# Performance work log

Hardware: AMD Instinct MI355X
Metric: run time of the kernel (lower is better)

Reference implementation:

```python
import jax, jax.numpy as jnp
import numpy as np

N_NODES = 100000
N_EDGES = 1600000
HID = 32


def gcn_conv(x, W, b, src, dst, num_nodes):
    # PyG GCNConv: h = X W; out = D^{-1/2}(A+I)D^{-1/2} h + b
    # (self loops already appended to src/dst by caller)
    h = x @ W
    deg = jax.ops.segment_sum(jnp.ones_like(dst, dtype=h.dtype), dst,
                              num_segments=num_nodes)
    dinv = jnp.where(deg > 0, jax.lax.rsqrt(deg), 0.0)
    norm = dinv[src] * dinv[dst]                      # [E+N]
    msg = h[src] * norm[:, None]                      # gather + scale
    out = jax.ops.segment_sum(msg, dst, num_segments=num_nodes)  # scatter-add
    return out + b


def setup_inputs() -> dict:
    key = jax.random.key(0)
    ks = jax.random.split(key, 12)
    x = jax.random.normal(ks[0], (N_NODES, 2), dtype=jnp.float32)
    edge_index = jax.random.randint(ks[1], (2, N_EDGES), 0, N_NODES,
                                    dtype=jnp.int32)
    s = 0.2  # small init scale
    return {
        "x": x,
        "edge_index": edge_index,
        "fc1_W": jax.random.normal(ks[2], (2, HID), jnp.float32) * s,
        "fc1_b": jnp.zeros((HID,), jnp.float32),
        "c1_W": jax.random.normal(ks[3], (HID, HID), jnp.float32) * s,
        "c1_b": jnp.zeros((HID,), jnp.float32),
        "c2_W": jax.random.normal(ks[4], (HID, HID), jnp.float32) * s,
        "c2_b": jnp.zeros((HID,), jnp.float32),
        "c3_W": jax.random.normal(ks[5], (HID, HID), jnp.float32) * s,
        "c3_b": jnp.zeros((HID,), jnp.float32),
        "fc2_W": jax.random.normal(ks[6], (HID, HID), jnp.float32) * s,
        "fc2_b": jnp.zeros((HID,), jnp.float32),
        "fc3_W": jax.random.normal(ks[7], (HID, 1), jnp.float32) * s,
        "fc3_b": jnp.zeros((1,), jnp.float32),
    }


def reference(x, edge_index, fc1_W, fc1_b, c1_W, c1_b, c2_W, c2_b,
              c3_W, c3_b, fc2_W, fc2_b, fc3_W, fc3_b):
    num_nodes = x.shape[0]
    loop = jnp.arange(num_nodes, dtype=edge_index.dtype)
    src = jnp.concatenate([edge_index[0], loop])  # add self loops
    dst = jnp.concatenate([edge_index[1], loop])
    h = jax.nn.relu(x @ fc1_W + fc1_b)
    h = jax.nn.relu(gcn_conv(h, c1_W, c1_b, src, dst, num_nodes))
    h = jax.nn.relu(gcn_conv(h, c2_W, c2_b, src, dst, num_nodes))
    h = jax.nn.relu(gcn_conv(h, c3_W, c3_b, src, dst, num_nodes))
    h = jax.nn.relu(h @ fc2_W + fc2_b)
    return h @ fc3_W + fc3_b
```

## Files before the change

kernel.cpp:

```cpp
#include <hip/hip_runtime.h>

#define NN 100000
#define NE 1600000
#define HID 32
#define NBK 391
#define CAP 4608
#define CHUNK 4096

__global__ __launch_bounds__(256) void partA_kernel(
        const int* __restrict__ src, const int* __restrict__ dst,
        int* __restrict__ bktcur, int* __restrict__ bedges) {
    __shared__ int cache[CHUNK];
    __shared__ int hist[NBK];
    __shared__ int lofs[NBK];
    int t = threadIdx.x;
    int base = blockIdx.x * CHUNK;
    for (int i = t; i < NBK; i += 256) hist[i] = 0;
    __syncthreads();
    for (int i = t; i < CHUNK; i += 256) {
        int e = base + i;
        if (e < NE) {
            int d = dst[e];
            cache[i] = d;
            atomicAdd(&hist[d >> 8], 1);
        }
    }
    __syncthreads();
    for (int i = t; i < NBK; i += 256)
        lofs[i] = hist[i] ? atomicAdd(&bktcur[i], hist[i]) : 0;
    __syncthreads();
    for (int i = t; i < CHUNK; i += 256) {
        int e = base + i;
        if (e < NE) {
            int d = cache[i];
            int s = src[e];
            int b = d >> 8;
            int rel = atomicAdd(&lofs[b], 1);
            if (rel < CAP) bedges[b * CAP + rel] = (s << 8) | (d & 255);
        }
    }
}

__global__ __launch_bounds__(256) void bucket_csr_fc1_kernel(
        const int* __restrict__ bedges, const int* __restrict__ bktcur,
        const float* __restrict__ x, const float* __restrict__ W1,
        const float* __restrict__ b1, float* __restrict__ dinv,
        int* __restrict__ srcidx, int* __restrict__ rbeg, int* __restrict__ rend,
        float* __restrict__ hs) {
    __shared__ int ldeg[256];
    __shared__ int lcur[256];
    __shared__ int wsum[256];
    __shared__ float sdinv[256];
    __shared__ float xs[512];
    __shared__ float wb[96];
    int b = blockIdx.x, t = threadIdx.x;
    int ebeg = b * CAP;
    int cnt = min(bktcur[b], CAP);
    int n0 = b << 8;
    ldeg[t] = 0;
    if (t < 96) wb[t] = (t < 64) ? W1[t] : b1[t - 64];
    for (int i = t; i < 512; i += 256) {
        int gi = 2 * n0 + i;
        xs[i] = (gi < 2 * NN) ? x[gi] : 0.f;
    }
    __syncthreads();
    for (int e = t; e < cnt; e += 256)
        atomicAdd(&ldeg[bedges[ebeg + e] & 255], 1);
    __syncthreads();
    int a = ldeg[t];
    wsum[t] = a;
    __syncthreads();
    for (int off = 1; off < 256; off <<= 1) {
        int xv = (t >= off) ? wsum[t - off] : 0;
        __syncthreads();
        wsum[t] += xv;
        __syncthreads();
    }
    int excl = wsum[t] - a;
    lcur[t] = excl;
    float dv = rsqrtf((float)(a + 1));
    sdinv[t] = dv;
    int n = n0 + t;
    if (n < NN) {
        rbeg[n] = ebeg + excl;
        rend[n] = ebeg + excl + a;
        dinv[n] = dv;
    }
    __syncthreads();
    for (int e = t; e < cnt; e += 256) {
        int w = bedges[ebeg + e];
        int pos = atomicAdd(&lcur[w & 255], 1);
        srcidx[ebeg + pos] = (unsigned)w >> 8;
    }
    int j = t & 31;
#pragma unroll
    for (int r = 0; r < 32; ++r) {
        int ln = (t >> 5) + (r << 3);
        int nn = n0 + ln;
        if (nn < NN) {
            float v = xs[2 * ln] * wb[j] + xs[2 * ln + 1] * wb[32 + j] + wb[64 + j];
            hs[(nn << 5) + j] = fmaxf(v, 0.f) * sdinv[ln];
        }
    }
}

template <bool OUTSCALE>
__global__ void conv_fused_kernel(const float* __restrict__ hs_in,
                                  const int* __restrict__ rbeg,
                                  const int* __restrict__ rend,
                                  const int* __restrict__ srcidx,
                                  const float* __restrict__ dinv,
                                  const float* __restrict__ W,
                                  const float* __restrict__ bias,
                                  float* __restrict__ hs_out) {
    __shared__ float wl[HID * HID];
    __shared__ float agg[8][HID];
    int tid = threadIdx.x;
    int base8 = blockIdx.x * 8;
#pragma unroll
    for (int i = 0; i < 4; ++i) wl[tid + 256 * i] = W[tid + 256 * i];
    int wave = tid >> 6, lane = tid & 63;
    int g = lane >> 3;
    int l = lane & 7;
#pragma unroll
    for (int rep = 0; rep < 2; ++rep) {
        int ln = wave * 2 + rep;
        int n = base8 + ln;
        int beg = rbeg[n], end = rend[n];
        float4 acc0 = make_float4(0.f, 0.f, 0.f, 0.f);
        float4 acc1 = make_float4(0.f, 0.f, 0.f, 0.f);
        int e = beg + g;
        for (; e + 8 < end; e += 16) {
            int s0 = srcidx[e];
            int s1 = srcidx[e + 8];
            float4 v0 = *(const float4*)&hs_in[(s0 << 5) + (l << 2)];
            float4 v1 = *(const float4*)&hs_in[(s1 << 5) + (l << 2)];
            acc0.x += v0.x; acc0.y += v0.y; acc0.z += v0.z; acc0.w += v0.w;
            acc1.x += v1.x; acc1.y += v1.y; acc1.z += v1.z; acc1.w += v1.w;
        }
        if (e < end) {
            int s0 = srcidx[e];
            float4 v0 = *(const float4*)&hs_in[(s0 << 5) + (l << 2)];
            acc0.x += v0.x; acc0.y += v0.y; acc0.z += v0.z; acc0.w += v0.w;
        }
        acc0.x += acc1.x; acc0.y += acc1.y; acc0.z += acc1.z; acc0.w += acc1.w;
#pragma unroll
        for (int m = 8; m < 64; m <<= 1) {
            acc0.x += __shfl_xor(acc0.x, m);
            acc0.y += __shfl_xor(acc0.y, m);
            acc0.z += __shfl_xor(acc0.z, m);
            acc0.w += __shfl_xor(acc0.w, m);
        }
        if (g == 0) {
            float4 self = *(const float4*)&hs_in[(n << 5) + (l << 2)];
            float dv = dinv[n];
            float4 r;
            r.x = (acc0.x + self.x) * dv;
            r.y = (acc0.y + self.y) * dv;
            r.z = (acc0.z + self.z) * dv;
            r.w = (acc0.w + self.w) * dv;
            *(float4*)&agg[ln][l << 2] = r;
        }
    }
    __syncthreads();
    int ln = tid >> 5, j = tid & 31;
    int n = base8 + ln;
    float v = 0.f;
#pragma unroll
    for (int k = 0; k < HID; ++k) v += agg[ln][k] * wl[k * HID + j];
    v = fmaxf(v + bias[j], 0.f);
    if (OUTSCALE) v *= dinv[n];
    hs_out[(n << 5) + j] = v;
}

__global__ void fc23_kernel(const float* __restrict__ h, const float* __restrict__ W2,
                            const float* __restrict__ b2, const float* __restrict__ W3,
                            const float* __restrict__ b3, float* __restrict__ out) {
    __shared__ float wl[HID * HID];
    __shared__ float hsl[256];
    int tid = threadIdx.x;
    int base = blockIdx.x * 256;
#pragma unroll
    for (int i = 0; i < 4; ++i) wl[tid + 256 * i] = W2[tid + 256 * i];
    hsl[tid] = h[base + tid];
    __syncthreads();
    int ln = tid >> 5, j = tid & 31;
    float v = 0.f;
#pragma unroll
    for (int k = 0; k < HID; ++k) v += hsl[ln * HID + k] * wl[k * HID + j];
    v = fmaxf(v + b2[j], 0.f);
    float p = v * W3[j];
#pragma unroll
    for (int m = 16; m; m >>= 1) p += __shfl_xor(p, m);
    if (j == 0) out[(base >> 5) + ln] = p + b3[0];
}

extern "C" void kernel_launch(void* const* d_in, const int* in_sizes, int n_in,
                              void* d_out, int out_size, void* d_ws, size_t ws_size,
                              hipStream_t stream) {
    const float* x     = (const float*)d_in[0];
    const int*   ei    = (const int*)d_in[1];
    const float* fc1_W = (const float*)d_in[2];
    const float* fc1_b = (const float*)d_in[3];
    const float* c1_W  = (const float*)d_in[4];
    const float* c1_b  = (const float*)d_in[5];
    const float* c2_W  = (const float*)d_in[6];
    const float* c2_b  = (const float*)d_in[7];
    const float* c3_W  = (const float*)d_in[8];
    const float* c3_b  = (const float*)d_in[9];
    const float* fc2_W = (const float*)d_in[10];
    const float* fc2_b = (const float*)d_in[11];
    const float* fc3_W = (const float*)d_in[12];
    const float* fc3_b = (const float*)d_in[13];

    const int* src = ei;
    const int* dst = ei + NE;

    float* ws     = (float*)d_ws;
    float* dinv   = ws;
    float* hA     = ws + NN;
    float* hB     = hA + NN * HID;
    int*   srcidx = (int*)(hB + NN * HID);
    int*   rbeg   = srcidx + NBK * CAP;
    int*   rend   = rbeg + NN;
    int*   bktcur = rend + NN;
    int*   bedges = (int*)hB;

    float* out = (float*)d_out;

    const int B = 256;
    const int gNH = (NN * HID) / B;
    const int gPart = (NE + CHUNK - 1) / CHUNK;

    hipMemsetAsync(bktcur, 0, NBK * sizeof(int), stream);
    partA_kernel<<<gPart, B, 0, stream>>>(src, dst, bktcur, bedges);
    bucket_csr_fc1_kernel<<<NBK, B, 0, stream>>>(bedges, bktcur, x, fc1_W, fc1_b,
                                                 dinv, srcidx, rbeg, rend, hA);

    conv_fused_kernel<true><<<gNH, B, 0, stream>>>(hA, rbeg, rend, srcidx, dinv, c1_W, c1_b, hB);
    conv_fused_kernel<true><<<gNH, B, 0, stream>>>(hB, rbeg, rend, srcidx, dinv, c2_W, c2_b, hA);
    conv_fused_kernel<false><<<gNH, B, 0, stream>>>(hA, rbeg, rend, srcidx, dinv, c3_W, c3_b, hB);

    fc23_kernel<<<gNH, B, 0, stream>>>(hB, fc2_W, fc2_b, fc3_W, fc3_b, out);
}
```

Before: 192.5 us.

## Fuse fc1 into first conv gather and fc2/fc3 into last conv

```diff
diff --git a/kernel.cpp b/kernel.cpp
--- a/kernel.cpp
+++ b/kernel.cpp
@@ -5,7 +5,7 @@
 #define HID 32
 #define NBK 391
 #define CAP 4608
-#define CHUNK 4096
+#define CHUNK 8192
 
 __global__ __launch_bounds__(256) void partA_kernel(
         const int* __restrict__ src, const int* __restrict__ dst,
@@ -41,28 +41,19 @@
     }
 }
 
-__global__ __launch_bounds__(256) void bucket_csr_fc1_kernel(
+__global__ __launch_bounds__(256) void bucket_csr_kernel(
         const int* __restrict__ bedges, const int* __restrict__ bktcur,
-        const float* __restrict__ x, const float* __restrict__ W1,
-        const float* __restrict__ b1, float* __restrict__ dinv,
+        const float* __restrict__ x, float* __restrict__ dinv,
         int* __restrict__ srcidx, int* __restrict__ rbeg, int* __restrict__ rend,
-        float* __restrict__ hs) {
+        float4* __restrict__ xpack) {
     __shared__ int ldeg[256];
     __shared__ int lcur[256];
     __shared__ int wsum[256];
-    __shared__ float sdinv[256];
-    __shared__ float xs[512];
-    __shared__ float wb[96];
     int b = blockIdx.x, t = threadIdx.x;
     int ebeg = b * CAP;
     int cnt = min(bktcur[b], CAP);
     int n0 = b << 8;
     ldeg[t] = 0;
-    if (t < 96) wb[t] = (t < 64) ? W1[t] : b1[t - 64];
-    for (int i = t; i < 512; i += 256) {
-        int gi = 2 * n0 + i;
-        xs[i] = (gi < 2 * NN) ? x[gi] : 0.f;
-    }
     __syncthreads();
     for (int e = t; e < cnt; e += 256)
         atomicAdd(&ldeg[bedges[ebeg + e] & 255], 1);
@@ -78,13 +69,14 @@
     }
     int excl = wsum[t] - a;
     lcur[t] = excl;
-    float dv = rsqrtf((float)(a + 1));
-    sdinv[t] = dv;
     int n = n0 + t;
     if (n < NN) {
+        float dv = rsqrtf((float)(a + 1));
         rbeg[n] = ebeg + excl;
         rend[n] = ebeg + excl + a;
         dinv[n] = dv;
+        float2 xv2 = *(const float2*)&x[2 * n];
+        xpack[n] = make_float4(xv2.x, xv2.y, dv, 0.f);
     }
     __syncthreads();
     for (int e = t; e < cnt; e += 256) {
@@ -92,19 +84,83 @@
         int pos = atomicAdd(&lcur[w & 255], 1);
         srcidx[ebeg + pos] = (unsigned)w >> 8;
     }
-    int j = t & 31;
-#pragma unroll
-    for (int r = 0; r < 32; ++r) {
-        int ln = (t >> 5) + (r << 3);
-        int nn = n0 + ln;
-        if (nn < NN) {
-            float v = xs[2 * ln] * wb[j] + xs[2 * ln + 1] * wb[32 + j] + wb[64 + j];
-            hs[(nn << 5) + j] = fmaxf(v, 0.f) * sdinv[ln];
-        }
-    }
-}
-
-template <bool OUTSCALE>
+}
+
+__global__ __launch_bounds__(256) void conv1_kernel(
+        const float4* __restrict__ xpack, const int* __restrict__ rbeg,
+        const int* __restrict__ rend, const int* __restrict__ srcidx,
+        const float* __restrict__ dinv, const float* __restrict__ W1,
+        const float* __restrict__ b1, const float* __restrict__ W,
+        const float* __restrict__ bias, float* __restrict__ hs_out) {
+    __shared__ float wl[HID * HID];
+    __shared__ float agg[8][HID];
+    int tid = threadIdx.x;
+    int base8 = blockIdx.x * 8;
+#pragma unroll
+    for (int i = 0; i < 4; ++i) wl[tid + 256 * i] = W[tid + 256 * i];
+    int wave = tid >> 6, lane = tid & 63;
+    int g = lane >> 3;
+    int l = lane & 7;
+    float4 w0q = *(const float4*)&W1[l << 2];
+    float4 w1q = *(const float4*)&W1[HID + (l << 2)];
+    float4 bq  = *(const float4*)&b1[l << 2];
+#pragma unroll
+    for (int rep = 0; rep < 2; ++rep) {
+        int ln = wave * 2 + rep;
+        int n = base8 + ln;
+        int beg = rbeg[n], end = rend[n];
+        float4 acc0 = make_float4(0.f, 0.f, 0.f, 0.f);
+        float4 acc1 = make_float4(0.f, 0.f, 0.f, 0.f);
+        int e = beg + g;
+        for (; e + 8 < end; e += 16) {
+            float4 p0 = xpack[srcidx[e]];
+            float4 p1 = xpack[srcidx[e + 8]];
+            acc0.x += fmaxf(p0.x * w0q.x + p0.y * w1q.x + bq.x, 0.f) * p0.z;
+            acc0.y += fmaxf(p0.x * w0q.y + p0.y * w1q.y + bq.y, 0.f) * p0.z;
+            acc0.z += fmaxf(p0.x * w0q.z + p0.y * w1q.z + bq.z, 0.f) * p0.z;
+            acc0.w += fmaxf(p0.x * w0q.w + p0.y * w1q.w + bq.w, 0.f) * p0.z;
+            acc1.x += fmaxf(p1.x * w0q.x + p1.y * w1q.x + bq.x, 0.f) * p1.z;
+            acc1.y += fmaxf(p1.x * w0q.y + p1.y * w1q.y + bq.y, 0.f) * p1.z;
+            acc1.z += fmaxf(p1.x * w0q.z + p1.y * w1q.z + bq.z, 0.f) * p1.z;
+            acc1.w += fmaxf(p1.x * w0q.w + p1.y * w1q.w + bq.w, 0.f) * p1.z;
+        }
+        if (e < end) {
+            float4 p0 = xpack[srcidx[e]];
+            acc0.x += fmaxf(p0.x * w0q.x + p0.y * w1q.x + bq.x, 0.f) * p0.z;
+            acc0.y += fmaxf(p0.x * w0q.y + p0.y * w1q.y + bq.y, 0.f) * p0.z;
+            acc0.z += fmaxf(p0.x * w0q.z + p0.y * w1q.z + bq.z, 0.f) * p0.z;
+            acc0.w += fmaxf(p0.x * w0q.w + p0.y * w1q.w + bq.w, 0.f) * p0.z;
+        }
+        acc0.x += acc1.x; acc0.y += acc1.y; acc0.z += acc1.z; acc0.w += acc1.w;
+#pragma unroll
+        for (int m = 8; m < 64; m <<= 1) {
+            acc0.x += __shfl_xor(acc0.x, m);
+            acc0.y += __shfl_xor(acc0.y, m);
+            acc0.z += __shfl_xor(acc0.z, m);
+            acc0.w += __shfl_xor(acc0.w, m);
+        }
+        if (g == 0) {
+            float4 ps = xpack[n];
+            float dv = ps.z;
+            float4 r;
+            r.x = (acc0.x + fmaxf(ps.x * w0q.x + ps.y * w1q.x + bq.x, 0.f) * dv) * dv;
+            r.y = (acc0.y + fmaxf(ps.x * w0q.y + ps.y * w1q.y + bq.y, 0.f) * dv) * dv;
+            r.z = (acc0.z + fmaxf(ps.x * w0q.z + ps.y * w1q.z + bq.z, 0.f) * dv) * dv;
+            r.w = (acc0.w + fmaxf(ps.x * w0q.w + ps.y * w1q.w + bq.w, 0.f) * dv) * dv;
+            *(float4*)&agg[ln][l << 2] = r;
+        }
+    }
+    __syncthreads();
+    int ln = tid >> 5, j = tid & 31;
+    int n = base8 + ln;
+    float v = 0.f;
+#pragma unroll
+    for (int k = 0; k < HID; ++k) v += agg[ln][k] * wl[k * HID + j];
+    v = fmaxf(v + bias[j], 0.f) * dinv[n];
+    hs_out[(n << 5) + j] = v;
+}
+
+template <bool OUTSCALE, bool FUSE23>
 __global__ void conv_fused_kernel(const float* __restrict__ hs_in,
                                   const int* __restrict__ rbeg,
                                   const int* __restrict__ rend,
@@ -112,6 +168,10 @@
                                   const float* __restrict__ dinv,
                                   const float* __restrict__ W,
                                   const float* __restrict__ bias,
+                                  const float* __restrict__ W2,
+                                  const float* __restrict__ b2,
+                                  const float* __restrict__ W3,
+                                  const float* __restrict__ b3,
                                   float* __restrict__ hs_out) {
     __shared__ float wl[HID * HID];
     __shared__ float agg[8][HID];
@@ -170,29 +230,23 @@
     for (int k = 0; k < HID; ++k) v += agg[ln][k] * wl[k * HID + j];
     v = fmaxf(v + bias[j], 0.f);
     if (OUTSCALE) v *= dinv[n];
-    hs_out[(n << 5) + j] = v;
-}
-
-__global__ void fc23_kernel(const float* __restrict__ h, const float* __restrict__ W2,
-                            const float* __restrict__ b2, const float* __restrict__ W3,
-                            const float* __restrict__ b3, float* __restrict__ out) {
-    __shared__ float wl[HID * HID];
-    __shared__ float hsl[256];
-    int tid = threadIdx.x;
-    int base = blockIdx.x * 256;
-#pragma unroll
-    for (int i = 0; i < 4; ++i) wl[tid + 256 * i] = W2[tid + 256 * i];
-    hsl[tid] = h[base + tid];
-    __syncthreads();
-    int ln = tid >> 5, j = tid & 31;
-    float v = 0.f;
-#pragma unroll
-    for (int k = 0; k < HID; ++k) v += hsl[ln * HID + k] * wl[k * HID + j];
-    v = fmaxf(v + b2[j], 0.f);
-    float p = v * W3[j];
-#pragma unroll
-    for (int m = 16; m; m >>= 1) p += __shfl_xor(p, m);
-    if (j == 0) out[(base >> 5) + ln] = p + b3[0];
+    if (!FUSE23) {
+        hs_out[(n << 5) + j] = v;
+    } else {
+        __syncthreads();
+#pragma unroll
+        for (int i = 0; i < 4; ++i) wl[tid + 256 * i] = W2[tid + 256 * i];
+        agg[ln][j] = v;
+        __syncthreads();
+        float v2 = 0.f;
+#pragma unroll
+        for (int k = 0; k < HID; ++k) v2 += agg[ln][k] * wl[k * HID + j];
+        v2 = fmaxf(v2 + b2[j], 0.f);
+        float p = v2 * W3[j];
+#pragma unroll
+        for (int m = 16; m; m >>= 1) p += __shfl_xor(p, m);
+        if (j == 0) hs_out[n] = p + b3[0];
+    }
 }
 
 extern "C" void kernel_launch(void* const* d_in, const int* in_sizes, int n_in,
@@ -216,15 +270,16 @@
     const int* src = ei;
     const int* dst = ei + NE;
 
-    float* ws     = (float*)d_ws;
-    float* dinv   = ws;
-    float* hA     = ws + NN;
-    float* hB     = hA + NN * HID;
-    int*   srcidx = (int*)(hB + NN * HID);
-    int*   rbeg   = srcidx + NBK * CAP;
-    int*   rend   = rbeg + NN;
-    int*   bktcur = rend + NN;
-    int*   bedges = (int*)hB;
+    float*  ws     = (float*)d_ws;
+    float*  dinv   = ws;
+    float*  hA     = ws + NN;
+    float*  hB     = hA + NN * HID;
+    float4* xpack  = (float4*)(hB + NN * HID);
+    int*    srcidx = (int*)(xpack + NN);
+    int*    rbeg   = srcidx + NBK * CAP;
+    int*    rend   = rbeg + NN;
+    int*    bktcur = rend + NN;
+    int*    bedges = (int*)hB;
 
     float* out = (float*)d_out;
 
@@ -234,12 +289,12 @@
 
     hipMemsetAsync(bktcur, 0, NBK * sizeof(int), stream);
     partA_kernel<<<gPart, B, 0, stream>>>(src, dst, bktcur, bedges);
-    bucket_csr_fc1_kernel<<<NBK, B, 0, stream>>>(bedges, bktcur, x, fc1_W, fc1_b,
-                                                 dinv, srcidx, rbeg, rend, hA);
-
-    conv_fused_kernel<true><<<gNH, B, 0, stream>>>(hA, rbeg, rend, srcidx, dinv, c1_W, c1_b, hB);
-    conv_fused_kernel<true><<<gNH, B, 0, stream>>>(hB, rbeg, rend, srcidx, dinv, c2_W, c2_b, hA);
-    conv_fused_kernel<false><<<gNH, B, 0, stream>>>(hA, rbeg, rend, srcidx, dinv, c3_W, c3_b, hB);
-
-    fc23_kernel<<<gNH, B, 0, stream>>>(hB, fc2_W, fc2_b, fc3_W, fc3_b, out);
-}
+    bucket_csr_kernel<<<NBK, B, 0, stream>>>(bedges, bktcur, x, dinv, srcidx, rbeg, rend, xpack);
+
+    conv1_kernel<<<gNH, B, 0, stream>>>(xpack, rbeg, rend, srcidx, dinv,
+                                        fc1_W, fc1_b, c1_W, c1_b, hB);
+    conv_fused_kernel<true, false><<<gNH, B, 0, stream>>>(
+        hB, rbeg, rend, srcidx, dinv, c2_W, c2_b, nullptr, nullptr, nullptr, nullptr, hA);
+    conv_fused_kernel<false, true><<<gNH, B, 0, stream>>>(
+        hA, rbeg, rend, srcidx, dinv, c3_W, c3_b, fc2_W, fc2_b, fc3_W, fc3_b, out);
+}
```

Measured after the change: 181.7 us. 5.6% less time.
